# Kernel tuning notes

Hardware: AMD Instinct MI355X
Metric: run time of the kernel (lower is better)

## Reference

```python
import jax, jax.numpy as jnp
import numpy as np

N_HEAD, D_HEAD, EMBED = 16, 64, 1024
B, Q_LEN, MEM_LEN = 2, 1024, 1024
K_LEN = Q_LEN + MEM_LEN  # == r_len
LN_EPS = 1e-3  # keras LayerNormalization default


def rel_shift(x):
    # x: [B, H, q, r]  (Transformer-XL relative shift)
    b, h, q, r = x.shape
    x = jnp.pad(x, ((0, 0), (0, 0), (0, 0), (1, 0)))
    x = x.reshape(b, h, r + 1, q)[:, :, 1:, :]
    return x.reshape(b, h, q, r)


def setup_inputs() -> dict:
    key = jax.random.key(0)
    ks = jax.random.split(key, 12)
    s = 0.02
    w = jax.random.normal(ks[0], (B, Q_LEN, EMBED), jnp.float32)
    r = jax.random.normal(ks[1], (K_LEN, EMBED), jnp.float32)
    member = jax.random.normal(ks[2], (B, MEM_LEN, EMBED), jnp.float32)
    r_w_bias = jax.random.normal(ks[3], (N_HEAD, D_HEAD), jnp.float32) * s
    r_r_bias = jax.random.normal(ks[4], (N_HEAD, D_HEAD), jnp.float32) * s
    # causal mask over [q_len, k_len]: position i may attend to mem + keys <= mem_len+i
    qi = jnp.arange(Q_LEN)[:, None]
    kj = jnp.arange(K_LEN)[None, :]
    attn_mask = (kj > qi + MEM_LEN).astype(jnp.float32)
    Wq = jax.random.normal(ks[5], (EMBED, N_HEAD * D_HEAD), jnp.float32) * s
    Wk = jax.random.normal(ks[6], (EMBED, N_HEAD * D_HEAD), jnp.float32) * s
    Wv = jax.random.normal(ks[7], (EMBED, N_HEAD * D_HEAD), jnp.float32) * s
    Wr = jax.random.normal(ks[8], (EMBED, N_HEAD * D_HEAD), jnp.float32) * s
    Wo = jax.random.normal(ks[9], (N_HEAD * D_HEAD, EMBED), jnp.float32) * s
    ln_gamma = jnp.ones((EMBED,), jnp.float32)
    ln_beta = jnp.zeros((EMBED,), jnp.float32)
    return {"w": w, "r": r, "attn_mask": attn_mask, "r_w_bias": r_w_bias,
            "r_r_bias": r_r_bias, "member": member, "Wq": Wq, "Wk": Wk,
            "Wv": Wv, "Wr": Wr, "Wo": Wo, "ln_gamma": ln_gamma, "ln_beta": ln_beta}


def reference(w, r, attn_mask, r_w_bias, r_r_bias, member, Wq, Wk, Wv, Wr, Wo, ln_gamma, ln_beta):
    b, q_len, _ = w.shape
    cat = jnp.concatenate([member, w], axis=1)          # [B, klen, D]
    klen = cat.shape[1]
    q = (cat @ Wq)[:, -q_len:].reshape(b, q_len, N_HEAD, D_HEAD)
    k = (cat @ Wk).reshape(b, klen, N_HEAD, D_HEAD)
    v = (cat @ Wv).reshape(b, klen, N_HEAD, D_HEAD)
    rr = (r @ Wr).reshape(r.shape[0], N_HEAD, D_HEAD)    # [rlen, H, dh]
    rw_q = q + r_w_bias[None, None]                      # content bias
    rr_q = q + r_r_bias[None, None]                      # position bias
    AC = jnp.einsum('bqhd,bkhd->bhqk', rw_q, k)
    BD = jnp.einsum('bqhd,rhd->bhqr', rr_q, rr)
    BD = rel_shift(BD)
    attn = (AC + BD) / jnp.sqrt(jnp.float32(EMBED))      # note: sqrt(embed), as in source
    m = attn_mask[None, None]                            # [1,1,q,k]
    attn = attn * (1.0 - m) - 1e30 * m
    score = jax.nn.softmax(attn, axis=-1)
    out = jnp.einsum('bhqk,bkhd->bqhd', score, v).reshape(b, q_len, N_HEAD * D_HEAD)
    out = out @ Wo
    x = w + out
    mu = jnp.mean(x, axis=-1, keepdims=True)
    var = jnp.mean(jnp.square(x - mu), axis=-1, keepdims=True)
    return (x - mu) * jax.lax.rsqrt(var + LN_EPS) * ln_gamma + ln_beta
```

## Files before the change

kernel.cpp:

```cpp
#include <hip/hip_runtime.h>


typedef __bf16 bf16;
typedef __bf16 bf16x4 __attribute__((ext_vector_type(4)));
typedef __bf16 bf16x8 __attribute__((ext_vector_type(8)));
typedef float f32x4 __attribute__((ext_vector_type(4)));

#define MFMA16(a, b, c) __builtin_amdgcn_mfma_f32_16x16x32_bf16((a), (b), (c), 0, 0, 0)

constexpr int E = 1024;
constexpr int NH = 16;
constexpr int DH = 64;
constexpr int QL = 1024;
constexpr int ML = 1024;
constexpr int KLEN = 2048;

__device__ __forceinline__ void ldg2lds16(const bf16* g, bf16* l) {
    __builtin_amdgcn_global_load_lds(
        (const __attribute__((address_space(1))) unsigned int*)g,
        (__attribute__((address_space(3))) unsigned int*)l, 16, 0, 0);
}

__device__ __forceinline__ bf16x8 frag8(const bf16* t, int row, int ch) {
    return *(const bf16x8*)(t + row * 64 + ((ch ^ (row & 7)) << 3));
}

__global__ void prep_k(const float* __restrict__ member, const float* __restrict__ w,
                       bf16* __restrict__ cat) {
    int row = blockIdx.x;
    int b = row >> 11, jj = row & 2047;
    const float* src = (jj < ML) ? member + ((size_t)(b * ML + jj)) * E
                                 : w + ((size_t)(b * QL + (jj - ML))) * E;
    float4 f = *(const float4*)(src + threadIdx.x * 4);
    bf16x4 o;
    o[0] = (bf16)f.x; o[1] = (bf16)f.y; o[2] = (bf16)f.z; o[3] = (bf16)f.w;
    *(bf16x4*)(cat + (size_t)row * E + threadIdx.x * 4) = o;
}

__global__ void transpose_k(const float* __restrict__ Wq, const float* __restrict__ Wk,
                            const float* __restrict__ Wv, const float* __restrict__ Wr,
                            const float* __restrict__ Wo, bf16* __restrict__ WqT,
                            bf16* __restrict__ WkT, bf16* __restrict__ WvT,
                            bf16* __restrict__ WrT, bf16* __restrict__ WoT) {
    const float* W; bf16* WT;
    switch (blockIdx.z) {
        case 0: W = Wq; WT = WqT; break;
        case 1: W = Wk; WT = WkT; break;
        case 2: W = Wv; WT = WvT; break;
        case 3: W = Wr; WT = WrT; break;
        default: W = Wo; WT = WoT; break;
    }
    __shared__ float t[32][33];
    int bx = blockIdx.x * 32, by = blockIdx.y * 32;
    int x = threadIdx.x, y = threadIdx.y;
    for (int yy = y; yy < 32; yy += 8)
        t[yy][x] = W[(by + yy) * E + bx + x];
    __syncthreads();
    for (int yy = y; yy < 32; yy += 8)
        WT[(bx + yy) * E + by + x] = (bf16)t[x][yy];
}

__global__ __launch_bounds__(256) void proj_k(
    const bf16* __restrict__ cat, const float* __restrict__ r,
    const bf16* __restrict__ WqT, const bf16* __restrict__ WkT,
    const bf16* __restrict__ WvT, const bf16* __restrict__ WrT,
    const float* __restrict__ rwb, const float* __restrict__ rrb,
    bf16* __restrict__ Qw, bf16* __restrict__ Qr, bf16* __restrict__ Kh,
    bf16* __restrict__ Vt, bf16* __restrict__ RRh) {
    __shared__ __align__(16) bf16 As[128 * 64];
    __shared__ __align__(16) bf16 Bs[128 * 64];
    const int tid = threadIdx.x;
    const int wave = tid >> 6, lane = tid & 63, quad = lane >> 4, l16 = lane & 15;

    int id = blockIdx.x, zone, base;
    if (id < 128) { zone = 0; base = 0; }
    else if (id < 384) { zone = 1; base = 128; }
    else if (id < 640) { zone = 2; base = 384; }
    else { zone = 3; base = 640; }
    const int lid = id - base;
    const int bn = (lid & 7) * 128, bm = (lid >> 3) * 128;
    const bf16* Bt = (zone == 0) ? WqT : (zone == 1) ? WkT : (zone == 2) ? WvT : WrT;
    const int wm = (wave >> 1) * 64, wn = (wave & 1) * 64;

    f32x4 acc[4][4] = {};

    for (int kk = 0; kk < E; kk += 64) {
        if (zone == 3) {
            int srw = tid >> 3, cch = tid & 7;
            for (int c = 0; c < 4; ++c) {
                int row = c * 32 + srw;
                const float* ap = r + (size_t)(bm + row) * E + kk + cch * 8;
                float4 f0 = *(const float4*)ap;
                float4 f1 = *(const float4*)(ap + 4);
                bf16x8 v;
                v[0] = (bf16)f0.x; v[1] = (bf16)f0.y; v[2] = (bf16)f0.z; v[3] = (bf16)f0.w;
                v[4] = (bf16)f1.x; v[5] = (bf16)f1.y; v[6] = (bf16)f1.z; v[7] = (bf16)f1.w;
                *(bf16x8*)(As + row * 64 + ((cch ^ (row & 7)) << 3)) = v;
            }
        } else {
            for (int issue = 0; issue < 4; ++issue) {
                int q = (issue * 4 + wave) * 64 + lane;
                int row = q >> 3, cs = (q & 7) ^ ((q >> 3) & 7);
                int gm = bm + row;
                const bf16* ap;
                if (zone == 0) {
                    int b = gm >> 10;
                    ap = cat + ((size_t)(b * 2048 + 1024 + (gm & 1023))) * E;
                } else {
                    ap = cat + (size_t)gm * E;
                }
                ldg2lds16(ap + kk + cs * 8, As + (issue * 4 + wave) * 512);
            }
        }
        for (int issue = 0; issue < 4; ++issue) {
            int q = (issue * 4 + wave) * 64 + lane;
            int row = q >> 3, cs = (q & 7) ^ ((q >> 3) & 7);
            ldg2lds16(Bt + (size_t)(bn + row) * E + kk + cs * 8,
                      Bs + (issue * 4 + wave) * 512);
        }
        __syncthreads();
        for (int ks = 0; ks < 64; ks += 32) {
            bf16x8 af[4], bfr[4];
            for (int mt = 0; mt < 4; ++mt)
                af[mt] = frag8(As, wm + mt * 16 + l16, (ks >> 3) + quad);
            for (int nt = 0; nt < 4; ++nt)
                bfr[nt] = frag8(Bs, wn + nt * 16 + l16, (ks >> 3) + quad);
            for (int mt = 0; mt < 4; ++mt)
                for (int nt = 0; nt < 4; ++nt)
                    acc[mt][nt] = MFMA16(af[mt], bfr[nt], acc[mt][nt]);
        }
        __syncthreads();
    }

    if (zone == 2) {
        bf16* buf = ((wave < 2) ? As : Bs) + (wave & 1) * 4096;
        for (int mt = 0; mt < 4; ++mt)
            for (int nt = 0; nt < 4; ++nt)
                for (int rr = 0; rr < 4; ++rr) {
                    int lr = mt * 16 + quad * 4 + rr;
                    int lc = nt * 16 + l16;
                    buf[lr * 64 + (((lc >> 3) ^ (lr & 7)) << 3) + (lc & 7)] =
                        (bf16)acc[mt][nt][rr];
                }
        int h = (bn + wn) >> 6;
        int gmw = bm + wm;
        int b = gmw >> 11, jb = gmw & 2047;
        for (int dp = 0; dp < 8; ++dp) {
            int dl = dp * 8 + (lane >> 3);
            int jl = (lane & 7) * 8;
            bf16x8 tmp;
            for (int jj = 0; jj < 8; ++jj) {
                int rw = jl + jj;
                tmp[jj] = buf[rw * 64 + (((dl >> 3) ^ (rw & 7)) << 3) + (dl & 7)];
            }
            *(bf16x8*)(Vt + (((size_t)(b * NH + h) * DH + dl) * KLEN) + jb + jl) = tmp;
        }
        return;
    }

    for (int mt = 0; mt < 4; ++mt)
        for (int nt = 0; nt < 4; ++nt)
            for (int rr = 0; rr < 4; ++rr) {
                int row = bm + wm + mt * 16 + quad * 4 + rr;
                int col = bn + wn + nt * 16 + l16;
                float v = acc[mt][nt][rr];
                if (zone == 0) {
                    int b = row >> 10, i = row & 1023;
                    int h = col >> 6, d = col & 63;
                    size_t o = (((size_t)(b * NH + h) * QL) + i) * DH + d;
                    Qw[o] = (bf16)((v + rwb[col]) * 0.03125f);
                    Qr[o] = (bf16)((v + rrb[col]) * 0.03125f);
                } else if (zone == 1) {
                    int b = row >> 11, j = row & 2047;
                    int h = col >> 6, d = col & 63;
                    Kh[(((size_t)(b * NH + h) * KLEN) + j) * DH + d] = (bf16)v;
                } else {
                    int h = col >> 6, d = col & 63;
                    RRh[(((size_t)h * KLEN) + row) * DH + d] = (bf16)v;
                }
            }
}

__global__ __launch_bounds__(256) void attn_k(
    const bf16* __restrict__ Qw, const bf16* __restrict__ Qr,
    const bf16* __restrict__ Kh, const bf16* __restrict__ Vt,
    const bf16* __restrict__ RRh, bf16* __restrict__ AttO) {
    __shared__ __align__(16) bf16 Ks[2][64 * 64];
    __shared__ __align__(16) bf16 Vs[2][64 * 64];
    __shared__ __align__(16) bf16 RRing[3][64 * 64];
    __shared__ __align__(16) bf16 UB[4][16 * 88];

    const int tid = threadIdx.x;
    const int wave = tid >> 6, lane = tid & 63, quad = lane >> 4, l16 = lane & 15;
    const int id = blockIdx.x;
    const int b = id >> 8, h = (id >> 4) & 15;
    const int qt = (id < 256) ? (id & 15) : (15 - (id & 15));
    const int i0 = qt * 64;

    const bf16* Qwb = Qw + ((size_t)(b * NH + h) * QL) * DH;
    const bf16* Qrb = Qr + ((size_t)(b * NH + h) * QL) * DH;
    const bf16* Kb = Kh + ((size_t)(b * NH + h) * KLEN) * DH;
    const bf16* Vb = Vt + ((size_t)(b * NH + h) * DH) * KLEN;
    const bf16* Rb = RRh + ((size_t)h * KLEN) * DH;

    bf16x8 qw0, qw1, qr0, qr1;
    {
        int i = i0 + wave * 16 + l16;
        qw0 = *(const bf16x8*)(Qwb + (size_t)i * DH + quad * 8);
        qw1 = *(const bf16x8*)(Qwb + (size_t)i * DH + 32 + quad * 8);
        qr0 = *(const bf16x8*)(Qrb + (size_t)i * DH + quad * 8);
        qr1 = *(const bf16x8*)(Qrb + (size_t)i * DH + 32 + quad * 8);
    }

    float lpart[4] = {0.f, 0.f, 0.f, 0.f};
    f32x4 oacc[4] = {};

    const int ntiles = qt + 17;
    const int cbase = 15 - qt;
    const int ptbase = 3 - wave;

    auto stage_kv = [&](int t) {
        const int j0 = t * 64;
        bf16* Kd = Ks[t & 1];
        bf16* Vd = Vs[t & 1];
        for (int issue = 0; issue < 2; ++issue) {
            int q = (issue * 4 + wave) * 64 + lane;
            int row = q >> 3, cs = (q & 7) ^ ((q >> 3) & 7);
            ldg2lds16(Kb + (size_t)(j0 + row) * DH + cs * 8,
                      Kd + (issue * 4 + wave) * 512);
            ldg2lds16(Vb + (size_t)row * KLEN + j0 + cs * 8,
                      Vd + (issue * 4 + wave) * 512);
        }
    };
    auto stage_rr = [&](int c) {
        bf16* Rd = RRing[c % 3];
        for (int issue = 0; issue < 2; ++issue) {
            int q = (issue * 4 + wave) * 64 + lane;
            int row = q >> 3, cs = (q & 7) ^ ((q >> 3) & 7);
            int pr = c * 64 + row;
            pr = pr > KLEN - 1 ? KLEN - 1 : pr;
            ldg2lds16(Rb + (size_t)pr * DH + cs * 8, Rd + (issue * 4 + wave) * 512);
        }
    };

    stage_kv(0);
    stage_rr(cbase);
    stage_rr(cbase + 1);
    __syncthreads();

    for (int t = 0; t < ntiles; ++t) {
        const bf16* Kt = Ks[t & 1];
        const bf16* Vl = Vs[t & 1];
        const bf16* Rlo = RRing[(cbase + t) % 3];
        const bf16* Rhi = RRing[(cbase + t + 1) % 3];
        if (t + 1 < ntiles) {
            stage_kv(t + 1);
            stage_rr(cbase + t + 2);
        }

        for (int pi = 0; pi < 5; ++pi) {
            int pt = ptbase + pi;
            const bf16* Rsrc = (pt < 4) ? Rlo : Rhi;
            int rrow = (pt & 3) * 16 + l16;
            f32x4 bacc = {};
            bacc = MFMA16(qr0, frag8(Rsrc, rrow, quad), bacc);
            bacc = MFMA16(qr1, frag8(Rsrc, rrow, 4 + quad), bacc);
            for (int rr = 0; rr < 4; ++rr)
                UB[wave][(quad * 4 + rr) * 88 + pi * 16 + l16] = (bf16)bacc[rr];
        }

        f32x4 sacc[4];
        for (int nt = 0; nt < 4; ++nt) {
            f32x4 a = {};
            a = MFMA16(qw0, frag8(Kt, nt * 16 + l16, quad), a);
            a = MFMA16(qw1, frag8(Kt, nt * 16 + l16, 4 + quad), a);
            sacc[nt] = a;
        }

        float sv[4][4];
        const bool lastt = (t == ntiles - 1);
        for (int nt = 0; nt < 4; ++nt)
            for (int rr = 0; rr < 4; ++rr) {
                int lr = quad * 4 + rr;
                int col = nt * 16 + l16 + 15 - lr;
                float bdv = (float)UB[wave][lr * 88 + col];
                float p = __expf(sacc[nt][rr] + bdv);
                if (lastt) {
                    int i = i0 + wave * 16 + lr;
                    int j = t * 64 + nt * 16 + l16;
                    if (j > i + ML) p = 0.f;
                }
                sv[nt][rr] = p;
                lpart[rr] += p;
            }

        for (int nt = 0; nt < 4; ++nt)
            for (int rr = 0; rr < 4; ++rr)
                UB[wave][(quad * 4 + rr) * 88 + nt * 16 + l16] = (bf16)sv[nt][rr];

        for (int c = 0; c < 2; ++c) {
            bf16x8 pa = *(const bf16x8*)(&UB[wave][l16 * 88 + c * 32 + quad * 8]);
            for (int nt = 0; nt < 4; ++nt) {
                bf16x8 vb = frag8(Vl, nt * 16 + l16, c * 4 + quad);
                oacc[nt] = MFMA16(pa, vb, oacc[nt]);
            }
        }
        __syncthreads();
    }

    float linv[4];
    for (int rr = 0; rr < 4; ++rr) {
        float v = lpart[rr];
        v += __shfl_xor(v, 1);
        v += __shfl_xor(v, 2);
        v += __shfl_xor(v, 4);
        v += __shfl_xor(v, 8);
        linv[rr] = 1.f / v;
    }

    for (int nt = 0; nt < 4; ++nt)
        for (int rr = 0; rr < 4; ++rr) {
            int i = i0 + wave * 16 + quad * 4 + rr;
            int d = nt * 16 + l16;
            AttO[((size_t)(b * QL + i)) * E + h * DH + d] =
                (bf16)(oacc[nt][rr] * linv[rr]);
        }
}

__global__ __launch_bounds__(256) void gemm_o(
    const bf16* __restrict__ A, const bf16* __restrict__ Bt,
    float* __restrict__ Xp) {
    __shared__ __align__(16) bf16 As[128 * 64];
    __shared__ __align__(16) bf16 Bs[128 * 64];
    const int tid = threadIdx.x;
    const int wave = tid >> 6, lane = tid & 63, quad = lane >> 4, l16 = lane & 15;
    const int bm = blockIdx.y * 128, bn = blockIdx.x * 128;
    const int kbase = blockIdx.z * 512;
    const int wm = (wave >> 1) * 64, wn = (wave & 1) * 64;

    f32x4 acc[4][4] = {};

    for (int s = 0; s < 8; ++s) {
        const int kk = kbase + s * 64;
        for (int issue = 0; issue < 4; ++issue) {
            int q = (issue * 4 + wave) * 64 + lane;
            int row = q >> 3, cs = (q & 7) ^ ((q >> 3) & 7);
            ldg2lds16(A + (size_t)(bm + row) * E + kk + cs * 8,
                      As + (issue * 4 + wave) * 512);
            ldg2lds16(Bt + (size_t)(bn + row) * E + kk + cs * 8,
                      Bs + (issue * 4 + wave) * 512);
        }
        __syncthreads();
        for (int ks = 0; ks < 64; ks += 32) {
            bf16x8 af[4], bfr[4];
            for (int mt = 0; mt < 4; ++mt)
                af[mt] = frag8(As, wm + mt * 16 + l16, (ks >> 3) + quad);
            for (int nt = 0; nt < 4; ++nt)
                bfr[nt] = frag8(Bs, wn + nt * 16 + l16, (ks >> 3) + quad);
            for (int mt = 0; mt < 4; ++mt)
                for (int nt = 0; nt < 4; ++nt)
                    acc[mt][nt] = MFMA16(af[mt], bfr[nt], acc[mt][nt]);
        }
        __syncthreads();
    }

    float* Xz = Xp + (size_t)blockIdx.z * 2048 * 1024;
    for (int mt = 0; mt < 4; ++mt)
        for (int nt = 0; nt < 4; ++nt)
            for (int rr = 0; rr < 4; ++rr) {
                int row = bm + wm + mt * 16 + quad * 4 + rr;
                int col = bn + wn + nt * 16 + l16;
                Xz[(size_t)row * E + col] = acc[mt][nt][rr];
            }
}

__global__ __launch_bounds__(256) void ln_k(const float* __restrict__ Xp,
                                            const float* __restrict__ resid,
                                            const float* __restrict__ gamma,
                                            const float* __restrict__ beta,
                                            float* __restrict__ out) {
    const int row = blockIdx.x;
    const int tid = threadIdx.x;
    const float* x0 = Xp + (size_t)row * E;
    const float* x1 = Xp + (size_t)2048 * 1024 + (size_t)row * E;
    const float* xr = resid + (size_t)row * E;
    float xv[4], s = 0.f, q = 0.f;
    for (int c = 0; c < 4; ++c) {
        int col = c * 256 + tid;
        float v = x0[col] + x1[col] + xr[col];
        xv[c] = v;
        s += v;
        q += v * v;
    }
    for (int off = 32; off > 0; off >>= 1) {
        s += __shfl_down(s, off);
        q += __shfl_down(q, off);
    }
    __shared__ float rs[4], rq[4];
    int wave = tid >> 6, lane = tid & 63;
    if (lane == 0) { rs[wave] = s; rq[wave] = q; }
    __syncthreads();
    float S = rs[0] + rs[1] + rs[2] + rs[3];
    float Q = rq[0] + rq[1] + rq[2] + rq[3];
    float mean = S * (1.f / E);
    float var = fmaxf(Q * (1.f / E) - mean * mean, 0.f);
    float rstd = rsqrtf(var + 1e-3f);
    for (int c = 0; c < 4; ++c) {
        int col = c * 256 + tid;
        out[(size_t)row * E + col] =
            (xv[c] - mean) * rstd * gamma[col] + beta[col];
    }
}

extern "C" void kernel_launch(void* const* d_in, const int* in_sizes, int n_in,
                              void* d_out, int out_size, void* d_ws,
                              size_t ws_size, hipStream_t stream) {
    (void)in_sizes; (void)n_in; (void)out_size; (void)ws_size;
    const float* w = (const float*)d_in[0];
    const float* r = (const float*)d_in[1];
    const float* rwb = (const float*)d_in[3];
    const float* rrb = (const float*)d_in[4];
    const float* member = (const float*)d_in[5];
    const float* Wq = (const float*)d_in[6];
    const float* Wk = (const float*)d_in[7];
    const float* Wv = (const float*)d_in[8];
    const float* Wr = (const float*)d_in[9];
    const float* Wo = (const float*)d_in[10];
    const float* gamma = (const float*)d_in[11];
    const float* beta = (const float*)d_in[12];
    float* out = (float*)d_out;

    char* ws = (char*)d_ws;
    const size_t MB = 1024 * 1024;
    bf16* WqT = (bf16*)(ws + 0 * MB);
    bf16* WkT = (bf16*)(ws + 2 * MB);
    bf16* WvT = (bf16*)(ws + 4 * MB);
    bf16* WrT = (bf16*)(ws + 6 * MB);
    bf16* WoT = (bf16*)(ws + 8 * MB);
    bf16* cat = (bf16*)(ws + 10 * MB);
    bf16* AttO = (bf16*)(ws + 14 * MB);
    bf16* Qw = (bf16*)(ws + 18 * MB);
    bf16* Qr = (bf16*)(ws + 22 * MB);
    float* Xp = (float*)(ws + 18 * MB);
    bf16* Kh = (bf16*)(ws + 26 * MB);
    bf16* Vt = (bf16*)(ws + 34 * MB);
    bf16* RRh = (bf16*)(ws + 42 * MB);

    prep_k<<<4096, 256, 0, stream>>>(member, w, cat);
    transpose_k<<<dim3(32, 32, 5), dim3(32, 8), 0, stream>>>(
        Wq, Wk, Wv, Wr, Wo, WqT, WkT, WvT, WrT, WoT);

    proj_k<<<768, 256, 0, stream>>>(cat, r, WqT, WkT, WvT, WrT, rwb, rrb, Qw,
                                    Qr, Kh, Vt, RRh);

    attn_k<<<512, 256, 0, stream>>>(Qw, Qr, Kh, Vt, RRh, AttO);

    gemm_o<<<dim3(8, 16, 2), 256, 0, stream>>>(AttO, WoT, Xp);
    ln_k<<<2048, 256, 0, stream>>>(Xp, w, gamma, beta, out);
}
```

Baseline: 261.8 us.

## Register-prefetch next K tile in projection and output GEMMs to overlap loads with MFMA

Replaces direct global-to-LDS loads in the QKV/R projection GEMM and the output GEMM with a register-staged pipeline. The next K slice is loaded into registers while MFMAs run on the current LDS tile, then written to LDS after a barrier. It also hoists per-thread address and swizzle computation out of the K loop. This aims to hide global memory latency behind compute, at the cost of more VGPRs (which may lower occupancy) and an extra LDS write per element instead of asynchronous direct-to-LDS loads.

```diff
diff --git a/kernel.cpp b/kernel.cpp
--- a/kernel.cpp
+++ b/kernel.cpp
@@ -84,41 +84,67 @@
 
     f32x4 acc[4][4] = {};
 
-    for (int kk = 0; kk < E; kk += 64) {
+    int srow[4], scs[4];
+    const bf16* arow[4];
+    for (int issue = 0; issue < 4; ++issue) {
+        int q = (issue * 4 + wave) * 64 + lane;
+        srow[issue] = q >> 3;
+        scs[issue] = (q & 7) ^ ((q >> 3) & 7);
+        int gm = bm + srow[issue];
+        if (zone == 0) {
+            int b = gm >> 10;
+            arow[issue] = cat + ((size_t)(b * 2048 + 1024 + (gm & 1023))) * E;
+        } else {
+            arow[issue] = cat + (size_t)gm * E;
+        }
+    }
+    const int z3row = tid >> 3, z3c = tid & 7;
+
+    bf16x8 rA[4], rB[4];
+    float4 zf0[4], zf1[4];
+
+    auto loadRegs = [&](int s) {
+        const int kk = s * 64;
         if (zone == 3) {
-            int srw = tid >> 3, cch = tid & 7;
             for (int c = 0; c < 4; ++c) {
-                int row = c * 32 + srw;
-                const float* ap = r + (size_t)(bm + row) * E + kk + cch * 8;
-                float4 f0 = *(const float4*)ap;
-                float4 f1 = *(const float4*)(ap + 4);
+                int row = c * 32 + z3row;
+                const float* ap = r + (size_t)(bm + row) * E + kk + z3c * 8;
+                zf0[c] = *(const float4*)ap;
+                zf1[c] = *(const float4*)(ap + 4);
+            }
+        } else {
+            for (int issue = 0; issue < 4; ++issue)
+                rA[issue] = *(const bf16x8*)(arow[issue] + kk + scs[issue] * 8);
+        }
+        for (int issue = 0; issue < 4; ++issue)
+            rB[issue] = *(const bf16x8*)(Bt + (size_t)(bn + srow[issue]) * E + kk +
+                                         scs[issue] * 8);
+    };
+    auto writeLDS = [&]() {
+        if (zone == 3) {
+            for (int c = 0; c < 4; ++c) {
+                int row = c * 32 + z3row;
                 bf16x8 v;
-                v[0] = (bf16)f0.x; v[1] = (bf16)f0.y; v[2] = (bf16)f0.z; v[3] = (bf16)f0.w;
-                v[4] = (bf16)f1.x; v[5] = (bf16)f1.y; v[6] = (bf16)f1.z; v[7] = (bf16)f1.w;
-                *(bf16x8*)(As + row * 64 + ((cch ^ (row & 7)) << 3)) = v;
+                v[0] = (bf16)zf0[c].x; v[1] = (bf16)zf0[c].y;
+                v[2] = (bf16)zf0[c].z; v[3] = (bf16)zf0[c].w;
+                v[4] = (bf16)zf1[c].x; v[5] = (bf16)zf1[c].y;
+                v[6] = (bf16)zf1[c].z; v[7] = (bf16)zf1[c].w;
+                *(bf16x8*)(As + row * 64 + ((z3c ^ (row & 7)) << 3)) = v;
             }
         } else {
-            for (int issue = 0; issue < 4; ++issue) {
-                int q = (issue * 4 + wave) * 64 + lane;
-                int row = q >> 3, cs = (q & 7) ^ ((q >> 3) & 7);
-                int gm = bm + row;
-                const bf16* ap;
-                if (zone == 0) {
-                    int b = gm >> 10;
-                    ap = cat + ((size_t)(b * 2048 + 1024 + (gm & 1023))) * E;
-                } else {
-                    ap = cat + (size_t)gm * E;
-                }
-                ldg2lds16(ap + kk + cs * 8, As + (issue * 4 + wave) * 512);
-            }
-        }
-        for (int issue = 0; issue < 4; ++issue) {
-            int q = (issue * 4 + wave) * 64 + lane;
-            int row = q >> 3, cs = (q & 7) ^ ((q >> 3) & 7);
-            ldg2lds16(Bt + (size_t)(bn + row) * E + kk + cs * 8,
-                      Bs + (issue * 4 + wave) * 512);
-        }
+            for (int issue = 0; issue < 4; ++issue)
+                *(bf16x8*)(As + (issue * 4 + wave) * 512 + lane * 8) = rA[issue];
+        }
+        for (int issue = 0; issue < 4; ++issue)
+            *(bf16x8*)(Bs + (issue * 4 + wave) * 512 + lane * 8) = rB[issue];
+    };
+
+    loadRegs(0);
+    for (int s = 0; s < 16; ++s) {
         __syncthreads();
+        writeLDS();
+        __syncthreads();
+        if (s + 1 < 16) loadRegs(s + 1);
         for (int ks = 0; ks < 64; ks += 32) {
             bf16x8 af[4], bfr[4];
             for (int mt = 0; mt < 4; ++mt)
@@ -129,10 +155,10 @@
                 for (int nt = 0; nt < 4; ++nt)
                     acc[mt][nt] = MFMA16(af[mt], bfr[nt], acc[mt][nt]);
         }
+    }
+
+    if (zone == 2) {
         __syncthreads();
-    }
-
-    if (zone == 2) {
         bf16* buf = ((wave < 2) ? As : Bs) + (wave & 1) * 4096;
         for (int mt = 0; mt < 4; ++mt)
             for (int nt = 0; nt < 4; ++nt)
@@ -340,17 +366,35 @@
 
     f32x4 acc[4][4] = {};
 
-    for (int s = 0; s < 8; ++s) {
+    int srow[4], scs[4];
+    for (int issue = 0; issue < 4; ++issue) {
+        int q = (issue * 4 + wave) * 64 + lane;
+        srow[issue] = q >> 3;
+        scs[issue] = (q & 7) ^ ((q >> 3) & 7);
+    }
+    bf16x8 rA[4], rB[4];
+    auto loadRegs = [&](int s) {
         const int kk = kbase + s * 64;
         for (int issue = 0; issue < 4; ++issue) {
-            int q = (issue * 4 + wave) * 64 + lane;
-            int row = q >> 3, cs = (q & 7) ^ ((q >> 3) & 7);
-            ldg2lds16(A + (size_t)(bm + row) * E + kk + cs * 8,
-                      As + (issue * 4 + wave) * 512);
-            ldg2lds16(Bt + (size_t)(bn + row) * E + kk + cs * 8,
-                      Bs + (issue * 4 + wave) * 512);
-        }
+            rA[issue] =
+                *(const bf16x8*)(A + (size_t)(bm + srow[issue]) * E + kk + scs[issue] * 8);
+            rB[issue] =
+                *(const bf16x8*)(Bt + (size_t)(bn + srow[issue]) * E + kk + scs[issue] * 8);
+        }
+    };
+    auto writeLDS = [&]() {
+        for (int issue = 0; issue < 4; ++issue) {
+            *(bf16x8*)(As + (issue * 4 + wave) * 512 + lane * 8) = rA[issue];
+            *(bf16x8*)(Bs + (issue * 4 + wave) * 512 + lane * 8) = rB[issue];
+        }
+    };
+
+    loadRegs(0);
+    for (int s = 0; s < 8; ++s) {
         __syncthreads();
+        writeLDS();
+        __syncthreads();
+        if (s + 1 < 8) loadRegs(s + 1);
         for (int ks = 0; ks < 64; ks += 32) {
             bf16x8 af[4], bfr[4];
             for (int mt = 0; mt < 4; ++mt)
@@ -361,7 +405,6 @@
                 for (int nt = 0; nt < 4; ++nt)
                     acc[mt][nt] = MFMA16(af[mt], bfr[nt], acc[mt][nt]);
         }
-        __syncthreads();
     }
 
     float* Xz = Xp + (size_t)blockIdx.z * 2048 * 1024;
```

Result: slower. 520.5 us (+98.9%).

## Fuse K and V projections sharing A tiles; merge prep and transpose kernels

Applied to the files above, without the earlier changes.

The K and V projection tiles now share one block. The block loads the cat A-tile once and keeps two accumulator sets, one against WkT and one against WvT, which halves A-tile global traffic for those zones and cuts the grid from 768 to 512 blocks. The separate weight-transpose and input-conversion kernels are merged into one launch to save a kernel launch. In exchange, the fused blocks need more LDS (a third 16KB buffer) and double the accumulator registers, which may lower occupancy and leave 256 heavy blocks unevenly balanced against the lighter ones.

```diff
diff --git a/kernel.cpp b/kernel.cpp
--- a/kernel.cpp
+++ b/kernel.cpp
@@ -25,39 +25,43 @@
     return *(const bf16x8*)(t + row * 64 + ((ch ^ (row & 7)) << 3));
 }
 
-__global__ void prep_k(const float* __restrict__ member, const float* __restrict__ w,
-                       bf16* __restrict__ cat) {
-    int row = blockIdx.x;
-    int b = row >> 11, jj = row & 2047;
-    const float* src = (jj < ML) ? member + ((size_t)(b * ML + jj)) * E
-                                 : w + ((size_t)(b * QL + (jj - ML))) * E;
-    float4 f = *(const float4*)(src + threadIdx.x * 4);
-    bf16x4 o;
-    o[0] = (bf16)f.x; o[1] = (bf16)f.y; o[2] = (bf16)f.z; o[3] = (bf16)f.w;
-    *(bf16x4*)(cat + (size_t)row * E + threadIdx.x * 4) = o;
-}
-
-__global__ void transpose_k(const float* __restrict__ Wq, const float* __restrict__ Wk,
-                            const float* __restrict__ Wv, const float* __restrict__ Wr,
-                            const float* __restrict__ Wo, bf16* __restrict__ WqT,
-                            bf16* __restrict__ WkT, bf16* __restrict__ WvT,
-                            bf16* __restrict__ WrT, bf16* __restrict__ WoT) {
-    const float* W; bf16* WT;
-    switch (blockIdx.z) {
-        case 0: W = Wq; WT = WqT; break;
-        case 1: W = Wk; WT = WkT; break;
-        case 2: W = Wv; WT = WvT; break;
-        case 3: W = Wr; WT = WrT; break;
-        default: W = Wo; WT = WoT; break;
-    }
+__global__ void pre_k(const float* __restrict__ Wq, const float* __restrict__ Wk,
+                      const float* __restrict__ Wv, const float* __restrict__ Wr,
+                      const float* __restrict__ Wo, const float* __restrict__ member,
+                      const float* __restrict__ w, bf16* __restrict__ WqT,
+                      bf16* __restrict__ WkT, bf16* __restrict__ WvT,
+                      bf16* __restrict__ WrT, bf16* __restrict__ WoT,
+                      bf16* __restrict__ cat) {
+    const int id = blockIdx.x;
+    const int tid = threadIdx.x;
     __shared__ float t[32][33];
-    int bx = blockIdx.x * 32, by = blockIdx.y * 32;
-    int x = threadIdx.x, y = threadIdx.y;
-    for (int yy = y; yy < 32; yy += 8)
-        t[yy][x] = W[(by + yy) * E + bx + x];
-    __syncthreads();
-    for (int yy = y; yy < 32; yy += 8)
-        WT[(bx + yy) * E + by + x] = (bf16)t[x][yy];
+    if (id < 5120) {
+        const float* W; bf16* WT;
+        switch (id >> 10) {
+            case 0: W = Wq; WT = WqT; break;
+            case 1: W = Wk; WT = WkT; break;
+            case 2: W = Wv; WT = WvT; break;
+            case 3: W = Wr; WT = WrT; break;
+            default: W = Wo; WT = WoT; break;
+        }
+        int xy = id & 1023;
+        int bx = (xy & 31) * 32, by = (xy >> 5) * 32;
+        int x = tid & 31, y = tid >> 5;
+        for (int yy = y; yy < 32; yy += 8)
+            t[yy][x] = W[(by + yy) * E + bx + x];
+        __syncthreads();
+        for (int yy = y; yy < 32; yy += 8)
+            WT[(bx + yy) * E + by + x] = (bf16)t[x][yy];
+    } else {
+        int row = id - 5120;
+        int b = row >> 11, jj = row & 2047;
+        const float* src = (jj < ML) ? member + ((size_t)(b * ML + jj)) * E
+                                     : w + ((size_t)(b * QL + (jj - ML))) * E;
+        float4 f = *(const float4*)(src + tid * 4);
+        bf16x4 o;
+        o[0] = (bf16)f.x; o[1] = (bf16)f.y; o[2] = (bf16)f.z; o[3] = (bf16)f.w;
+        *(bf16x4*)(cat + (size_t)row * E + tid * 4) = o;
+    }
 }
 
 __global__ __launch_bounds__(256) void proj_k(
@@ -69,23 +73,22 @@
     bf16* __restrict__ Vt, bf16* __restrict__ RRh) {
     __shared__ __align__(16) bf16 As[128 * 64];
     __shared__ __align__(16) bf16 Bs[128 * 64];
+    __shared__ __align__(16) bf16 Cs[128 * 64];
     const int tid = threadIdx.x;
     const int wave = tid >> 6, lane = tid & 63, quad = lane >> 4, l16 = lane & 15;
 
-    int id = blockIdx.x, zone, base;
-    if (id < 128) { zone = 0; base = 0; }
-    else if (id < 384) { zone = 1; base = 128; }
-    else if (id < 640) { zone = 2; base = 384; }
-    else { zone = 3; base = 640; }
-    const int lid = id - base;
+    const int id = blockIdx.x;
+    const int zone = (id < 256) ? 0 : (id < 384) ? 1 : 2;
+    const int lid = (zone == 0) ? id : (zone == 1) ? id - 256 : id - 384;
     const int bn = (lid & 7) * 128, bm = (lid >> 3) * 128;
-    const bf16* Bt = (zone == 0) ? WqT : (zone == 1) ? WkT : (zone == 2) ? WvT : WrT;
+    const bf16* Bt = (zone == 0) ? WkT : (zone == 1) ? WqT : WrT;
     const int wm = (wave >> 1) * 64, wn = (wave & 1) * 64;
 
     f32x4 acc[4][4] = {};
+    f32x4 acc2[4][4] = {};
 
     for (int kk = 0; kk < E; kk += 64) {
-        if (zone == 3) {
+        if (zone == 2) {
             int srw = tid >> 3, cch = tid & 7;
             for (int c = 0; c < 4; ++c) {
                 int row = c * 32 + srw;
@@ -103,7 +106,7 @@
                 int row = q >> 3, cs = (q & 7) ^ ((q >> 3) & 7);
                 int gm = bm + row;
                 const bf16* ap;
-                if (zone == 0) {
+                if (zone == 1) {
                     int b = gm >> 10;
                     ap = cat + ((size_t)(b * 2048 + 1024 + (gm & 1023))) * E;
                 } else {
@@ -117,6 +120,14 @@
             int row = q >> 3, cs = (q & 7) ^ ((q >> 3) & 7);
             ldg2lds16(Bt + (size_t)(bn + row) * E + kk + cs * 8,
                       Bs + (issue * 4 + wave) * 512);
+        }
+        if (zone == 0) {
+            for (int issue = 0; issue < 4; ++issue) {
+                int q = (issue * 4 + wave) * 64 + lane;
+                int row = q >> 3, cs = (q & 7) ^ ((q >> 3) & 7);
+                ldg2lds16(WvT + (size_t)(bn + row) * E + kk + cs * 8,
+                          Cs + (issue * 4 + wave) * 512);
+            }
         }
         __syncthreads();
         for (int ks = 0; ks < 64; ks += 32) {
@@ -128,11 +139,29 @@
             for (int mt = 0; mt < 4; ++mt)
                 for (int nt = 0; nt < 4; ++nt)
                     acc[mt][nt] = MFMA16(af[mt], bfr[nt], acc[mt][nt]);
-        }
-        __syncthreads();
-    }
-
-    if (zone == 2) {
+            if (zone == 0) {
+                bf16x8 cfr[4];
+                for (int nt = 0; nt < 4; ++nt)
+                    cfr[nt] = frag8(Cs, wn + nt * 16 + l16, (ks >> 3) + quad);
+                for (int mt = 0; mt < 4; ++mt)
+                    for (int nt = 0; nt < 4; ++nt)
+                        acc2[mt][nt] = MFMA16(af[mt], cfr[nt], acc2[mt][nt]);
+            }
+        }
+        __syncthreads();
+    }
+
+    if (zone == 0) {
+        for (int mt = 0; mt < 4; ++mt)
+            for (int nt = 0; nt < 4; ++nt)
+                for (int rr = 0; rr < 4; ++rr) {
+                    int row = bm + wm + mt * 16 + quad * 4 + rr;
+                    int col = bn + wn + nt * 16 + l16;
+                    int b = row >> 11, j = row & 2047;
+                    int h = col >> 6, d = col & 63;
+                    Kh[(((size_t)(b * NH + h) * KLEN) + j) * DH + d] =
+                        (bf16)acc[mt][nt][rr];
+                }
         bf16* buf = ((wave < 2) ? As : Bs) + (wave & 1) * 4096;
         for (int mt = 0; mt < 4; ++mt)
             for (int nt = 0; nt < 4; ++nt)
@@ -140,7 +169,7 @@
                     int lr = mt * 16 + quad * 4 + rr;
                     int lc = nt * 16 + l16;
                     buf[lr * 64 + (((lc >> 3) ^ (lr & 7)) << 3) + (lc & 7)] =
-                        (bf16)acc[mt][nt][rr];
+                        (bf16)acc2[mt][nt][rr];
                 }
         int h = (bn + wn) >> 6;
         int gmw = bm + wm;
@@ -164,16 +193,12 @@
                 int row = bm + wm + mt * 16 + quad * 4 + rr;
                 int col = bn + wn + nt * 16 + l16;
                 float v = acc[mt][nt][rr];
-                if (zone == 0) {
+                if (zone == 1) {
                     int b = row >> 10, i = row & 1023;
                     int h = col >> 6, d = col & 63;
                     size_t o = (((size_t)(b * NH + h) * QL) + i) * DH + d;
                     Qw[o] = (bf16)((v + rwb[col]) * 0.03125f);
                     Qr[o] = (bf16)((v + rrb[col]) * 0.03125f);
-                } else if (zone == 1) {
-                    int b = row >> 11, j = row & 2047;
-                    int h = col >> 6, d = col & 63;
-                    Kh[(((size_t)(b * NH + h) * KLEN) + j) * DH + d] = (bf16)v;
                 } else {
                     int h = col >> 6, d = col & 63;
                     RRh[(((size_t)h * KLEN) + row) * DH + d] = (bf16)v;
@@ -446,11 +471,10 @@
     bf16* Vt = (bf16*)(ws + 34 * MB);
     bf16* RRh = (bf16*)(ws + 42 * MB);
 
-    prep_k<<<4096, 256, 0, stream>>>(member, w, cat);
-    transpose_k<<<dim3(32, 32, 5), dim3(32, 8), 0, stream>>>(
-        Wq, Wk, Wv, Wr, Wo, WqT, WkT, WvT, WrT, WoT);
-
-    proj_k<<<768, 256, 0, stream>>>(cat, r, WqT, WkT, WvT, WrT, rwb, rrb, Qw,
+    pre_k<<<9216, 256, 0, stream>>>(Wq, Wk, Wv, Wr, Wo, member, w, WqT, WkT,
+                                    WvT, WrT, WoT, cat);
+
+    proj_k<<<512, 256, 0, stream>>>(cat, r, WqT, WkT, WvT, WrT, rwb, rrb, Qw,
                                     Qr, Kh, Vt, RRh);
 
     attn_k<<<512, 256, 0, stream>>>(Qw, Qr, Kh, Vt, RRh, AttO);
```

New measurement: 268.7 us. 1.03x slower.
